# Kernel optimization log

Hardware: AMD Instinct MI355X
Metric: run time of the kernel (lower is better)

Reference implementation:

```python
import jax, jax.numpy as jnp
import numpy as np

B, S, D, H = 128, 256, 256, 8   # graphs, nodes/graph, dim_h, heads
N = B * S
E = 524288
DH = D // H
BN_EPS = 1e-5

def _bn(v, g, b):
    # BatchNorm1d forward with batch statistics (biased var), eval-dropout model
    m = v.mean(0)
    var = v.var(0)
    return (v - m) * jax.lax.rsqrt(var + BN_EPS) * g + b

def setup_inputs() -> dict:
    key = jax.random.key(0)
    ks = jax.random.split(key, 40)
    x = jax.random.normal(ks[0], (N, D), jnp.float32)
    src = jax.random.randint(ks[1], (E,), 0, N)
    dst = (src // S) * S + jax.random.randint(ks[2], (E,), 0, S)  # intra-graph edges
    edge_index = jnp.stack([src, dst]).astype(jnp.int64)
    def lin(k, i, o):
        return (jax.random.normal(k, (i, o), jnp.float32) / np.float32(np.sqrt(i)))
    inp = {
        'x': x, 'edge_index': edge_index,
        'W_gcn': lin(ks[3], D, D), 'b_gcn': jnp.zeros((D,), jnp.float32),
        'W_gin1': lin(ks[4], D, D), 'b_gin1': jnp.zeros((D,), jnp.float32),
        'W_gin2': lin(ks[5], D, D), 'b_gin2': jnp.zeros((D,), jnp.float32),
        'g_kv': jnp.ones((D,), jnp.float32), 'be_kv': jnp.zeros((D,), jnp.float32),
        'Wq1': lin(ks[6], D, D), 'bq1': jnp.zeros((D,), jnp.float32),
        'Wq2': lin(ks[7], D, D), 'bq2': jnp.zeros((D,), jnp.float32),
        'Wq_a': lin(ks[8], D, D), 'bq_a': jnp.zeros((D,), jnp.float32),
        'Wk_a': lin(ks[9], D, D), 'bk_a': jnp.zeros((D,), jnp.float32),
        'Wv_a': lin(ks[10], D, D), 'bv_a': jnp.zeros((D,), jnp.float32),
        'Wo_a': lin(ks[11], D, D), 'bo_a': jnp.zeros((D,), jnp.float32),
        'g_attn': jnp.ones((D,), jnp.float32), 'be_attn': jnp.zeros((D,), jnp.float32),
        'Wf1': lin(ks[12], D, 2 * D), 'bf1': jnp.zeros((2 * D,), jnp.float32),
        'Wf2': lin(ks[13], 2 * D, D), 'bf2': jnp.zeros((D,), jnp.float32),
        'g2': jnp.ones((D,), jnp.float32), 'be2': jnp.zeros((D,), jnp.float32),
    }
    return inp

def _forward(x, edge_index,
             W_gcn, b_gcn, W_gin1, b_gin1, W_gin2, b_gin2, g_kv, be_kv,
             Wq1, bq1, Wq2, bq2,
             Wq_a, bq_a, Wk_a, bk_a, Wv_a, bv_a, Wo_a, bo_a, g_attn, be_attn,
             Wf1, bf1, Wf2, bf2, g2, be2):
    row, col = edge_index[0], edge_index[1]
    h_in1 = x

    # ---- expert 0: GCNConv (add self loops + symmetric norm) ----
    loops = jnp.arange(N, dtype=row.dtype)
    row2 = jnp.concatenate([row, loops])
    col2 = jnp.concatenate([col, loops])
    deg = jax.ops.segment_sum(jnp.ones_like(row2, jnp.float32), col2, num_segments=N)
    dinv = jnp.where(deg > 0, jax.lax.rsqrt(deg), 0.0)
    norm = dinv[row2] * dinv[col2]                     # [E+N]
    xw = x @ W_gcn                                      # [N, D]
    h_gcn = jax.ops.segment_sum(norm[:, None] * xw[row2], col2, num_segments=N) + b_gcn
    e0 = _bn(h_gcn, g_kv, be_kv)

    # ---- expert 1: GINConv (eps=0, sum aggregation, 2-layer MLP) ----
    agg = jax.ops.segment_sum(x[row], col, num_segments=N)
    h_gin = jax.nn.relu((x + agg) @ W_gin1 + b_gin1) @ W_gin2 + b_gin2
    e1 = _bn(h_gin, g_kv, be_kv)

    # ---- global expert normalization (torch .std -> unbiased) ----
    allo = jnp.concatenate([e0, e1], axis=0)
    gm = allo.mean()
    gs = jnp.std(allo, ddof=1)
    e0 = (e0 - gm) / (gs + 1e-8)
    e1 = (e1 - gm) / (gs + 1e-8)

    # ---- uniform routing & kv residual mix ----
    kv = 0.5 * e0 + 0.5 * e1 + 0.1 * h_in1              # [N, D]

    # ---- dense batching (equal-sized graphs -> pure reshape, full mask) ----
    q_dense = h_in1.reshape(B, S, D)
    kv_dense = kv.reshape(B, S, D)

    # ---- q projection MLP ----
    q_dense = jax.nn.relu(q_dense @ Wq1 + bq1) @ Wq2 + bq2

    # ---- multihead attention (batch_first, no padding) ----
    qh = (q_dense @ Wq_a + bq_a).reshape(B, S, H, DH)
    kh = (kv_dense @ Wk_a + bk_a).reshape(B, S, H, DH)
    vh = (kv_dense @ Wv_a + bv_a).reshape(B, S, H, DH)
    scores = jnp.einsum('bqhd,bkhd->bhqk', qh, kh) / np.float32(np.sqrt(DH))
    attn = jax.nn.softmax(scores, axis=-1)
    o = jnp.einsum('bhqk,bkhd->bqhd', attn, vh).reshape(B, S, D)
    h_attn = (o @ Wo_a + bo_a).reshape(N, D)

    # ---- residual + norm + FFN block ----
    h = _bn(h_in1 + h_attn, g_attn, be_attn)
    h_ff = jax.nn.relu(h @ Wf1 + bf1) @ Wf2 + bf2
    h = _bn(h + h_ff, g2, be2)
    return h

def reference(x, edge_index,
              W_gcn, b_gcn, W_gin1, b_gin1, W_gin2, b_gin2, g_kv, be_kv,
              Wq1, bq1, Wq2, bq2,
              Wq_a, bq_a, Wk_a, bk_a, Wv_a, bv_a, Wo_a, bo_a, g_attn, be_attn,
              Wf1, bf1, Wf2, bf2, g2, be2):
    return _forward(x, edge_index,
                    W_gcn, b_gcn, W_gin1, b_gin1, W_gin2, b_gin2, g_kv, be_kv,
                    Wq1, bq1, Wq2, bq2,
                    Wq_a, bq_a, Wk_a, bk_a, Wv_a, bv_a, Wo_a, bo_a, g_attn, be_attn,
                    Wf1, bf1, Wf2, bf2, g2, be2)
```

## Files before the change

### kernel.cpp

```cpp
#include <hip/hip_runtime.h>
#include <hip/hip_bf16.h>

typedef __hip_bfloat16 bf16;
typedef __attribute__((ext_vector_type(8))) short short8;
typedef __attribute__((ext_vector_type(4))) short short4v;
typedef __attribute__((ext_vector_type(4))) float f32x4;
typedef __attribute__((ext_vector_type(4))) int i32x4;

#define N_ 32768
#define D_ 256
#define S_ 256
#define B_ 128
#define E_ 524288

static __device__ __forceinline__ f32x4 mfma16(short8 a, short8 b, f32x4 c) {
  return __builtin_amdgcn_mfma_f32_16x16x32_bf16(a, b, c, 0, 0, 0);
}
static __device__ __forceinline__ f32x4 fzero4() {
  f32x4 z; z[0] = 0.f; z[1] = 0.f; z[2] = 0.f; z[3] = 0.f; return z;
}
static __device__ __forceinline__ float bits2f(short s) {
  unsigned u = ((unsigned)(unsigned short)s) << 16;
  return __builtin_bit_cast(float, u);
}
static __device__ __forceinline__ short f2bits(float f) {
  bf16 b = __float2bfloat16(f);
  return __builtin_bit_cast(short, b);
}
static __device__ __forceinline__ float tof(float x) { return x; }
static __device__ __forceinline__ float tof(bf16 x) { return __bfloat162float(x); }

#define GLOAD_LDS16(G, L) __builtin_amdgcn_global_load_lds( \
    (const __attribute__((address_space(1))) void*)(G),     \
    (__attribute__((address_space(3))) void*)(L), 16, 0, 0)

template<int F>
__global__ __launch_bounds__(256)
void gemm_bt(const bf16* __restrict__ A, const bf16* __restrict__ Bt,
             const float* __restrict__ bias, const float* __restrict__ biasB,
             const void* __restrict__ resid,
             float* __restrict__ Cf, bf16* __restrict__ Cb,
             float* __restrict__ Sp, float* __restrict__ SSp,
             int M, int Nc, int K, long bsA, long bsB, long bsC)
{
  __shared__ __align__(16) bf16 lA[128 * 32];
  __shared__ __align__(16) bf16 lB[128 * 32];
  __shared__ float sS[2][128], sSS[2][128];
  const int z = blockIdx.z;
  const bf16* Ab = A + (long)z * bsA;
  const bf16* Bb = Bt + (long)z * bsB;
  const int m0 = blockIdx.x * 128, n0 = blockIdx.y * 128;
  const int tid = threadIdx.x;
  const int lane = tid & 63;
  const int w = tid >> 6, wr = w >> 1, wc = w & 1;
  const int g = lane >> 4, r = lane & 15, ko = g * 8;
  const int srow = lane >> 2, skw = (lane & 3) * 8;

  f32x4 acc[4][4];
  for (int i = 0; i < 4; i++) for (int j = 0; j < 4; j++) acc[i][j] = fzero4();

  for (int k0 = 0; k0 < K; k0 += 32) {
    __syncthreads();
    for (int i = 0; i < 2; i++) {
      const int c = w * 2 + i;
      GLOAD_LDS16(Ab + (long)(m0 + c * 16 + srow) * K + k0 + skw, lA + c * 512);
      GLOAD_LDS16(Bb + (long)(n0 + c * 16 + srow) * K + k0 + skw, lB + c * 512);
    }
    __syncthreads();
    short8 af[4], bfv[4];
    for (int mi = 0; mi < 4; mi++)
      af[mi] = *(const short8*)&lA[(wr * 64 + mi * 16 + r) * 32 + ko];
    for (int ni = 0; ni < 4; ni++)
      bfv[ni] = *(const short8*)&lB[(wc * 64 + ni * 16 + r) * 32 + ko];
    for (int mi = 0; mi < 4; mi++)
      for (int ni = 0; ni < 4; ni++)
        acc[mi][ni] = mfma16(af[mi], bfv[ni], acc[mi][ni]);
  }

  float cs[4] = {0, 0, 0, 0}, css[4] = {0, 0, 0, 0};
  for (int mi = 0; mi < 4; mi++) for (int ni = 0; ni < 4; ni++) {
    const int row = m0 + wr * 64 + mi * 16 + g * 4;
    const int col = n0 + wc * 64 + ni * 16 + r;
    float bv = 0.0f;
    if (F & 2) {
      if ((F & 128) && col >= 256) bv = biasB[col - 256];
      else bv = bias[col];
    }
    for (int j = 0; j < 4; j++) {
      long idx = (long)(row + j) * Nc + col;
      float v = acc[mi][ni][j] + bv;
      if (F & 4)  v += ((const float*)resid)[(long)z * bsC + idx];
      if (F & 64) v += bits2f(((const short*)resid)[(long)z * bsC + idx]);
      if (F & 1)  v = fmaxf(v, 0.0f);
      if (F & 32) { cs[ni] += v; css[ni] += v * v; }
      if (F & 8)  Cf[(long)z * bsC + idx] = v;
      if (F & 16) Cb[(long)z * bsC + idx] = __float2bfloat16(v);
    }
  }
  if (F & 32) {
    for (int ni = 0; ni < 4; ni++) {
      cs[ni]  += __shfl_xor(cs[ni], 16);  cs[ni]  += __shfl_xor(cs[ni], 32);
      css[ni] += __shfl_xor(css[ni], 16); css[ni] += __shfl_xor(css[ni], 32);
    }
    if (lane < 16) {
      for (int ni = 0; ni < 4; ni++) {
        sS[wr][wc * 64 + ni * 16 + lane]  = cs[ni];
        sSS[wr][wc * 64 + ni * 16 + lane] = css[ni];
      }
    }
    __syncthreads();
    if (tid < 128) {
      atomicAdd(&Sp[n0 + tid],  sS[0][tid] + sS[1][tid]);
      atomicAdd(&SSp[n0 + tid], sSS[0][tid] + sSS[1][tid]);
    }
  }
}

template<int STAGES, bool STATS>
__global__ __launch_bounds__(512)
void mlp_fused(const bf16* __restrict__ A,
               const bf16* __restrict__ B1, const float* __restrict__ b1,
               const bf16* __restrict__ B2, const float* __restrict__ b2,
               const bf16* __restrict__ B3, const float* __restrict__ b3,
               bf16* __restrict__ C, float* __restrict__ Sp, float* __restrict__ SSp)
{
  __shared__ __align__(16) bf16 lA[64 * 32];
  __shared__ __align__(16) bf16 lB[256 * 32];
  __shared__ __align__(16) bf16 lC[64 * 256];
  char* lCc = (char*)lC;
  const int tid = threadIdx.x;
  const int lane = tid & 63;
  const int w = tid >> 6;
  const int mh = w >> 2, nq = w & 3;
  const int g = lane >> 4, r = lane & 15, ko = g * 8;
  const int m0 = blockIdx.x * 64;

  f32x4 acc[2][4];
  for (int i = 0; i < 2; i++) for (int j = 0; j < 4; j++) acc[i][j] = fzero4();

  for (int k0 = 0; k0 < 256; k0 += 32) {
    __syncthreads();
    if (tid < 256)
      GLOAD_LDS16(A + (long)(m0 + (tid >> 2)) * 256 + k0 + (tid & 3) * 8,
                  lA + w * 512);
    GLOAD_LDS16(B1 + (long)(tid >> 2) * 256 + k0 + (tid & 3) * 8,
                lB + w * 512);
    GLOAD_LDS16(B1 + (long)((tid + 512) >> 2) * 256 + k0 + ((tid + 512) & 3) * 8,
                lB + w * 512 + 4096);
    __syncthreads();
    short8 af[2], bfv[4];
    for (int mi = 0; mi < 2; mi++)
      af[mi] = *(const short8*)&lA[(mh * 32 + mi * 16 + r) * 32 + ko];
    for (int ni = 0; ni < 4; ni++)
      bfv[ni] = *(const short8*)&lB[(nq * 64 + ni * 16 + r) * 32 + ko];
    for (int mi = 0; mi < 2; mi++)
      for (int ni = 0; ni < 4; ni++)
        acc[mi][ni] = mfma16(af[mi], bfv[ni], acc[mi][ni]);
  }
  for (int mi = 0; mi < 2; mi++) for (int ni = 0; ni < 4; ni++) {
    const int col = nq * 64 + ni * 16 + r;
    const float bv = b1[col];
    for (int j = 0; j < 4; j++) {
      const int row = mh * 32 + mi * 16 + g * 4 + j;
      float v = fmaxf(acc[mi][ni][j] + bv, 0.0f);
      *(short*)(lCc + ((row * 512 + col * 2) ^ ((row & 7) << 4))) = f2bits(v);
    }
  }
  __syncthreads();

  const bf16* Bs = B2;
  for (int s = 1; s < STAGES; s++) {
    for (int i = 0; i < 2; i++) for (int j = 0; j < 4; j++) acc[i][j] = fzero4();
    for (int k0 = 0; k0 < 256; k0 += 32) {
      __syncthreads();
      GLOAD_LDS16(Bs + (long)(tid >> 2) * 256 + k0 + (tid & 3) * 8,
                  lB + w * 512);
      GLOAD_LDS16(Bs + (long)((tid + 512) >> 2) * 256 + k0 + ((tid + 512) & 3) * 8,
                  lB + w * 512 + 4096);
      __syncthreads();
      short8 af[2], bfv[4];
      for (int mi = 0; mi < 2; mi++) {
        const int row = mh * 32 + mi * 16 + r;
        af[mi] = *(const short8*)(lCc +
                  ((row * 512 + (k0 + ko) * 2) ^ ((row & 7) << 4)));
      }
      for (int ni = 0; ni < 4; ni++)
        bfv[ni] = *(const short8*)&lB[(nq * 64 + ni * 16 + r) * 32 + ko];
      for (int mi = 0; mi < 2; mi++)
        for (int ni = 0; ni < 4; ni++)
          acc[mi][ni] = mfma16(af[mi], bfv[ni], acc[mi][ni]);
    }
    if (s < STAGES - 1) {
      __syncthreads();
      for (int mi = 0; mi < 2; mi++) for (int ni = 0; ni < 4; ni++) {
        const int col = nq * 64 + ni * 16 + r;
        const float bv = b2[col];
        for (int j = 0; j < 4; j++) {
          const int row = mh * 32 + mi * 16 + g * 4 + j;
          float v = acc[mi][ni][j] + bv;
          *(short*)(lCc + ((row * 512 + col * 2) ^ ((row & 7) << 4))) = f2bits(v);
        }
      }
      __syncthreads();
      Bs = B3;
    }
  }

  const float* bf_ = (STAGES == 3) ? b3 : b2;
  float cs[4] = {0, 0, 0, 0}, css[4] = {0, 0, 0, 0};
  for (int mi = 0; mi < 2; mi++) for (int ni = 0; ni < 4; ni++) {
    const int col = nq * 64 + ni * 16 + r;
    const float bv = bf_[col];
    for (int j = 0; j < 4; j++) {
      const int row = mh * 32 + mi * 16 + g * 4 + j;
      float v = acc[mi][ni][j] + bv;
      if (STATS) { cs[ni] += v; css[ni] += v * v; }
      C[(long)(m0 + row) * 256 + col] = __float2bfloat16(v);
    }
  }
  if (STATS) {
    for (int ni = 0; ni < 4; ni++) {
      cs[ni]  += __shfl_xor(cs[ni], 16);  cs[ni]  += __shfl_xor(cs[ni], 32);
      css[ni] += __shfl_xor(css[ni], 16); css[ni] += __shfl_xor(css[ni], 32);
    }
    __syncthreads();
    float* sS = (float*)lC;
    if (lane < 16) {
      for (int ni = 0; ni < 4; ni++) {
        sS[mh * 256 + nq * 64 + ni * 16 + lane] = cs[ni];
        sS[512 + mh * 256 + nq * 64 + ni * 16 + lane] = css[ni];
      }
    }
    __syncthreads();
    if (tid < 256) {
      atomicAdd(&Sp[tid],  sS[tid] + sS[256 + tid]);
      atomicAdd(&SSp[tid], sS[512 + tid] + sS[768 + tid]);
    }
  }
}

__global__ __launch_bounds__(256, 2)
void attn_k(const bf16* __restrict__ qh, const bf16* __restrict__ kh,
            const bf16* __restrict__ vh, bf16* __restrict__ ob, int ks)
{
  const int h = blockIdx.x, qhf = blockIdx.y, b = blockIdx.z;
  const int tid = threadIdx.x, lane = tid & 63, w = tid >> 6;
  const int g = lane >> 4, r = lane & 15, ko = g * 8;
  __shared__ __align__(16) bf16 lK[256 * 32];
  __shared__ __align__(16) bf16 lV[32 * 256];
  char* lKc = (char*)lK;
  char* lVc = (char*)lV;

  for (int i = 0; i < 4; i++) {
    int c = tid + i * 256;
    int row = c >> 2, p4 = c & 3;
    short8 v = *(const short8*)(kh + (long)(b * 256 + row) * ks + h * 32 + p4 * 8);
    *(short8*)(lKc + ((row * 64 + p4 * 16) ^ ((row & 7) << 4))) = v;
  }
  for (int i = 0; i < 2; i++) {
    int c = tid + i * 256;
    int sp = c >> 2, part = c & 3;
    const bf16* vp = vh + (long)(b * 256 + 2 * sp) * ks + h * 32 + part * 8;
    short8 va = *(const short8*)(vp);
    short8 vb = *(const short8*)(vp + ks);
    #pragma unroll
    for (int j = 0; j < 8; j++) {
      int dh = part * 8 + j;
      int sw = ((dh & 7) ^ ((dh >> 3) << 1)) & 7;
      unsigned wrd = ((unsigned)(unsigned short)vb[j] << 16) |
                     (unsigned)(unsigned short)va[j];
      *(unsigned*)(lVc + ((dh * 512 + sp * 4) ^ (sw << 4))) = wrd;
    }
  }
  __syncthreads();

  const float c1 = 0.17677669529663687f * 1.4426950408889634f;
  const int idx0 = (((lane >> 4) & 1) * 32 + r) * 4;
  const int idx1 = idx0 + 64;
  const bool selhi = lane >= 32;

  for (int mc = 0; mc < 2; mc++) {
    const long qbase = (long)b * 256 + qhf * 128 + w * 32 + mc * 16;
    short8 qf = *(const short8*)(qh + (qbase + r) * 256 + h * 32 + ko);
    f32x4 sc[16];
    __builtin_amdgcn_s_setprio(1);
    #pragma unroll
    for (int nc = 0; nc < 16; nc++) {
      int row = nc * 16 + r;
      short8 kf = *(const short8*)(lKc + ((row * 64 + g * 16) ^ ((r & 7) << 4)));
      sc[nc] = mfma16(kf, qf, fzero4());
    }
    __builtin_amdgcn_s_setprio(0);
    f32x4 m4 = sc[0];
    #pragma unroll
    for (int nc = 1; nc < 16; nc++)
      for (int j = 0; j < 4; j++) m4[j] = fmaxf(m4[j], sc[nc][j]);
    float mx = fmaxf(fmaxf(m4[0], m4[1]), fmaxf(m4[2], m4[3]));
    mx = fmaxf(mx, __shfl_xor(mx, 16));
    mx = fmaxf(mx, __shfl_xor(mx, 32));
    const float mxc = mx * c1;
    f32x4 s4 = fzero4();
    #pragma unroll
    for (int nc = 0; nc < 16; nc++)
      for (int j = 0; j < 4; j++) {
        float p = exp2f(fmaf(sc[nc][j], c1, -mxc));
        sc[nc][j] = p; s4[j] += p;
      }
    float sum = s4[0] + s4[1] + s4[2] + s4[3];
    sum += __shfl_xor(sum, 16);
    sum += __shfl_xor(sum, 32);
    const float invs = 1.0f / sum;
    f32x4 oa[2]; oa[0] = fzero4(); oa[1] = fzero4();
    __builtin_amdgcn_s_setprio(1);
    #pragma unroll
    for (int kc = 0; kc < 8; kc++) {
      int pkA0, pkA1, pkB0, pkB1;
      {
        const f32x4 pa = sc[2 * kc], pb = sc[2 * kc + 1];
        unsigned a0 = (unsigned short)f2bits(pa[0] * invs);
        unsigned a1 = (unsigned short)f2bits(pa[1] * invs);
        unsigned a2 = (unsigned short)f2bits(pa[2] * invs);
        unsigned a3 = (unsigned short)f2bits(pa[3] * invs);
        unsigned b0 = (unsigned short)f2bits(pb[0] * invs);
        unsigned b1 = (unsigned short)f2bits(pb[1] * invs);
        unsigned b2 = (unsigned short)f2bits(pb[2] * invs);
        unsigned b3 = (unsigned short)f2bits(pb[3] * invs);
        pkA0 = (int)((a1 << 16) | a0);
        pkA1 = (int)((a3 << 16) | a2);
        pkB0 = (int)((b1 << 16) | b0);
        pkB1 = (int)((b3 << 16) | b2);
      }
      int A0 = __builtin_amdgcn_ds_bpermute(idx0, pkA0);
      int A1 = __builtin_amdgcn_ds_bpermute(idx0, pkA1);
      int B0 = __builtin_amdgcn_ds_bpermute(idx0, pkB0);
      int B1 = __builtin_amdgcn_ds_bpermute(idx0, pkB1);
      int C0 = __builtin_amdgcn_ds_bpermute(idx1, pkA0);
      int C1 = __builtin_amdgcn_ds_bpermute(idx1, pkA1);
      int D0 = __builtin_amdgcn_ds_bpermute(idx1, pkB0);
      int D1 = __builtin_amdgcn_ds_bpermute(idx1, pkB1);
      i32x4 av;
      av[0] = selhi ? B0 : A0;
      av[1] = selhi ? B1 : A1;
      av[2] = selhi ? D0 : C0;
      av[3] = selhi ? D1 : C1;
      short8 af = __builtin_bit_cast(short8, av);
      #pragma unroll
      for (int n = 0; n < 2; n++) {
        int dh = n * 16 + r;
        int sw = ((dh & 7) ^ ((dh >> 3) << 1)) & 7;
        short8 bv = *(const short8*)(lVc + ((dh * 512 + kc * 64 + g * 16) ^ (sw << 4)));
        oa[n] = mfma16(af, bv, oa[n]);
      }
    }
    __builtin_amdgcn_s_setprio(0);
    #pragma unroll
    for (int n = 0; n < 2; n++)
      for (int j = 0; j < 4; j++)
        ob[(qbase + g * 4 + j) * 256 + h * 32 + n * 16 + r] =
          __float2bfloat16(oa[n][j]);
  }
}

template<typename TIN>
__global__ __launch_bounds__(256)
void transpose_cast_k(const TIN* __restrict__ in, bf16* __restrict__ out,
                      int in_rs, int out_rs, long zhi, long out_zs)
{
  __shared__ float tile[32][33];
  const int z = blockIdx.z;
  const long ioff = (long)z * zhi;
  const long ooff = (long)z * out_zs;
  const int tx = threadIdx.x, ty = threadIdx.y;
  const int c = blockIdx.x * 32 + tx;
  const int rb = blockIdx.y * 32;
  for (int i = 0; i < 4; i++)
    tile[ty + i * 8][tx] = tof(in[ioff + (long)(rb + ty + i * 8) * in_rs + c]);
  __syncthreads();
  const int oc = rb + tx;
  const int orb = blockIdx.x * 32;
  for (int i = 0; i < 4; i++)
    out[ooff + (long)(orb + ty + i * 8) * out_rs + oc] =
      __float2bfloat16(tile[tx][ty + i * 8]);
}

__global__ __launch_bounds__(256)
void xprep_k(const float* __restrict__ x, bf16* __restrict__ xb,
             bf16* __restrict__ xT)
{
  __shared__ float tile[32][33];
  const int z = blockIdx.z;
  const long ioff = (long)z * 65536;
  const int tx = threadIdx.x, ty = threadIdx.y;
  const int c = blockIdx.x * 32 + tx;
  const int rb = blockIdx.y * 32;
  for (int i = 0; i < 4; i++) {
    float v = x[ioff + (long)(rb + ty + i * 8) * 256 + c];
    tile[ty + i * 8][tx] = v;
    xb[ioff + (long)(rb + ty + i * 8) * 256 + c] = __float2bfloat16(v);
  }
  __syncthreads();
  const int oc = rb + tx;
  const int orb = blockIdx.x * 32;
  for (int i = 0; i < 4; i++)
    xT[ioff + (long)(orb + ty + i * 8) * 256 + oc] =
      __float2bfloat16(tile[tx][ty + i * 8]);
}

__global__ __launch_bounds__(256)
void w9t_k(const float* w0, const float* w1, const float* w2, const float* w3,
           const float* w4, const float* w5, const float* w6, const float* w7,
           const float* w8, bf16* __restrict__ out)
{
  __shared__ float tile[32][33];
  const float* srcs[9] = {w0, w1, w2, w3, w4, w5, w6, w7, w8};
  const int wi = blockIdx.z;
  const float* in = srcs[wi];
  bf16* o = out + (long)wi * 65536;
  const int tx = threadIdx.x, ty = threadIdx.y;
  const int c = blockIdx.x * 32 + tx;
  const int rb = blockIdx.y * 32;
  for (int i = 0; i < 4; i++)
    tile[ty + i * 8][tx] = in[(rb + ty + i * 8) * 256 + c];
  __syncthreads();
  const int oc = rb + tx;
  const int orb = blockIdx.x * 32;
  for (int i = 0; i < 4; i++)
    o[(orb + ty + i * 8) * 256 + oc] = __float2bfloat16(tile[tx][ty + i * 8]);
}

__global__ __launch_bounds__(256)
void edge_cnt_k(const int* __restrict__ ei, unsigned* __restrict__ cnt)
{
  int e = blockIdx.x * 256 + threadIdx.x;
  int src = ei[e], dst = ei[E_ + e];
  long idx = ((long)(src >> 8) * 256 + (dst & 255)) * 256 + (src & 255);
  atomicAdd(&cnt[idx >> 2], 1u << ((idx & 3) * 8));
}

__global__ __launch_bounds__(256)
void deg_k(const unsigned* __restrict__ cnt, float* __restrict__ dinv)
{
  int rid = blockIdx.x * 16 + (threadIdx.x >> 4);
  int l16 = threadIdx.x & 15;
  uint4 v = ((const uint4*)(cnt + (long)rid * 64))[l16];
  unsigned s = 0;
  s += (v.x & 0xFF) + ((v.x >> 8) & 0xFF) + ((v.x >> 16) & 0xFF) + (v.x >> 24);
  s += (v.y & 0xFF) + ((v.y >> 8) & 0xFF) + ((v.y >> 16) & 0xFF) + (v.y >> 24);
  s += (v.z & 0xFF) + ((v.z >> 8) & 0xFF) + ((v.z >> 16) & 0xFF) + (v.z >> 24);
  s += (v.w & 0xFF) + ((v.w >> 8) & 0xFF) + ((v.w >> 16) & 0xFF) + (v.w >> 24);
  s += __shfl_xor(s, 1); s += __shfl_xor(s, 2);
  s += __shfl_xor(s, 4); s += __shfl_xor(s, 8);
  if (l16 == 0) dinv[rid] = rsqrtf((float)s + 1.0f);
}

__global__ __launch_bounds__(256)
void adj_derive_k(const unsigned* __restrict__ cnt, const float* __restrict__ dinv,
                  bf16* __restrict__ gin, bf16* __restrict__ gcn)
{
  long wi = (long)blockIdx.x * 256 + threadIdx.x;
  unsigned cw = cnt[wi];
  long i = wi * 4;
  float cv[4] = {(float)(cw & 0xFF), (float)((cw >> 8) & 0xFF),
                 (float)((cw >> 16) & 0xFF), (float)(cw >> 24)};
  long row = i >> 8;
  int g = (int)(row >> 8), dst = (int)(row & 255);
  int src0 = (int)(i & 255);
  float dd = dinv[row];
  const float* ds = dinv + (long)g * 256 + src0;
  short4v oi, oc;
  for (int j = 0; j < 4; j++) {
    float gv = cv[j] * dd * ds[j];
    if (src0 + j == dst) gv += dd * dd;
    oi[j] = f2bits(cv[j]);
    oc[j] = f2bits(gv);
  }
  *(short4v*)(gin + i) = oi;
  *(short4v*)(gcn + i) = oc;
}

__global__ __launch_bounds__(256)
void expert_stats_k(const float* __restrict__ S0, const float* __restrict__ SS0,
                    const float* __restrict__ S1, const float* __restrict__ SS1,
                    const float* __restrict__ gkv, const float* __restrict__ bkv,
                    float* __restrict__ kA, float* __restrict__ kB,
                    float* __restrict__ kC)
{
  const int d = threadIdx.x;
  const float invN = 1.0f / 32768.0f;
  float m0 = S0[d] * invN, v0 = SS0[d] * invN - m0 * m0;
  float a0 = gkv[d] * rsqrtf(v0 + 1e-5f), c0 = bkv[d] - m0 * a0;
  float m1 = S1[d] * invN, v1 = SS1[d] * invN - m1 * m1;
  float a1 = gkv[d] * rsqrtf(v1 + 1e-5f), c1 = bkv[d] - m1 * a1;
  float gsum = a0 * S0[d] + 32768.0f * c0 + a1 * S1[d] + 32768.0f * c1;
  float gss  = a0 * a0 * SS0[d] + 2.0f * a0 * c0 * S0[d] + 32768.0f * c0 * c0
             + a1 * a1 * SS1[d] + 2.0f * a1 * c1 * S1[d] + 32768.0f * c1 * c1;
  __shared__ float r1[256], r2[256];
  r1[d] = gsum; r2[d] = gss;
  __syncthreads();
  for (int s = 128; s > 0; s >>= 1) {
    if (d < s) { r1[d] += r1[d + s]; r2[d] += r2[d + s]; }
    __syncthreads();
  }
  const float cntall = 16777216.0f;
  float tg = r1[0], tss = r2[0];
  float gm = tg / cntall;
  float var = (tss - tg * tg / cntall) / (cntall - 1.0f);
  float gs = sqrtf(fmaxf(var, 0.f)) + 1e-8f;
  kA[d] = 0.5f * a0 / gs;
  kB[d] = 0.5f * a1 / gs;
  kC[d] = 0.5f * (c0 + c1 - 2.0f * gm) / gs;
}

__global__ __launch_bounds__(256)
void kv_mix_k(const bf16* __restrict__ hgcn, const bf16* __restrict__ hgin,
              const bf16* __restrict__ xb, const float* __restrict__ kA,
              const float* __restrict__ kB, const float* __restrict__ kC,
              bf16* __restrict__ kv)
{
  long i = ((long)blockIdx.x * 256 + threadIdx.x) * 8;
  int d0 = (int)(i & 255);
  short8 a = *(const short8*)(hgcn + i);
  short8 b = *(const short8*)(hgin + i);
  short8 c = *(const short8*)(xb + i);
  short8 o;
  for (int j = 0; j < 8; j++) {
    int d = d0 + j;
    float v = kA[d] * bits2f(a[j]) + kB[d] * bits2f(b[j]) + kC[d] + 0.1f * bits2f(c[j]);
    o[j] = f2bits(v);
  }
  *(short8*)(kv + i) = o;
}

template<int MODE>
__global__ __launch_bounds__(256)
void bn_apply_k(const bf16* __restrict__ in, const float* __restrict__ S,
                const float* __restrict__ SSq, const float* __restrict__ gg,
                const float* __restrict__ bb, float* __restrict__ outf,
                bf16* __restrict__ outb)
{
  long i = ((long)blockIdx.x * 256 + threadIdx.x) * 8;
  int d0 = (int)(i & 255);
  short8 v = *(const short8*)(in + i);
  const float invN = 1.0f / 32768.0f;
  float4 o0, o1; short8 o8;
  for (int j = 0; j < 8; j++) {
    int d = d0 + j;
    float m = S[d] * invN;
    float var = SSq[d] * invN - m * m;
    float a = gg[d] * rsqrtf(var + 1e-5f);
    float c = bb[d] - m * a;
    float o = a * bits2f(v[j]) + c;
    if (MODE & 1) { if (j < 4) (&o0.x)[j] = o; else (&o1.x)[j - 4] = o; }
    if (MODE & 2) o8[j] = f2bits(o);
  }
  if (MODE & 1) { *(float4*)(outf + i) = o0; *(float4*)(outf + i + 4) = o1; }
  if (MODE & 2) *(short8*)(outb + i) = o8;
}

static constexpr size_t OFF_S0 = 0, OFF_SS0 = 1024, OFF_S1 = 2048, OFF_SS1 = 3072;
static constexpr size_t OFF_S2 = 4096, OFF_SS2 = 5120, OFF_S3 = 6144, OFF_SS3 = 7168;
static constexpr size_t OFF_KA = 8192, OFF_KB = 9216, OFF_KC = 10240;
static constexpr size_t OFF_CNT = 16384;
static constexpr size_t CNT_BYTES = (size_t)B_ * S_ * S_;
static constexpr size_t ZERO_BYTES = OFF_CNT + CNT_BYTES;
static constexpr size_t OFF_DINV = OFF_CNT + (size_t)B_ * S_ * S_ * 2;
static constexpr size_t OFF_W = OFF_DINV + 131072;
static constexpr size_t NDB2 = (size_t)N_ * D_ * 2;
static constexpr size_t OFF_ADJGINB = OFF_W + 1703936;
static constexpr size_t OFF_ADJGCNB = OFF_ADJGINB + NDB2;
static constexpr size_t OFF_XB   = OFF_ADJGCNB + NDB2;
static constexpr size_t OFF_XT   = OFF_XB + NDB2;
static constexpr size_t OFF_AGG  = OFF_XT + NDB2;
static constexpr size_t OFF_GIN  = OFF_AGG + NDB2;
static constexpr size_t OFF_KV   = OFF_GIN + NDB2;
static constexpr size_t OFF_HGCN = OFF_KV + NDB2;
static constexpr size_t OFF_HGIN = OFF_HGCN + NDB2;

extern "C" void kernel_launch(void* const* d_in, const int* in_sizes, int n_in,
                              void* d_out, int out_size, void* d_ws, size_t ws_size,
                              hipStream_t stream)
{
  (void)in_sizes; (void)n_in; (void)out_size; (void)ws_size;
  const float* x      = (const float*)d_in[0];
  const int*   ei     = (const int*)d_in[1];
  const float* W_gcn  = (const float*)d_in[2];
  const float* b_gcn  = (const float*)d_in[3];
  const float* W_gin1 = (const float*)d_in[4];
  const float* b_gin1 = (const float*)d_in[5];
  const float* W_gin2 = (const float*)d_in[6];
  const float* b_gin2 = (const float*)d_in[7];
  const float* g_kv   = (const float*)d_in[8];
  const float* be_kv  = (const float*)d_in[9];
  const float* Wq1    = (const float*)d_in[10];
  const float* bq1    = (const float*)d_in[11];
  const float* Wq2    = (const float*)d_in[12];
  const float* bq2    = (const float*)d_in[13];
  const float* Wq_a   = (const float*)d_in[14];
  const float* bq_a   = (const float*)d_in[15];
  const float* Wk_a   = (const float*)d_in[16];
  const float* bk_a   = (const float*)d_in[17];
  const float* Wv_a   = (const float*)d_in[18];
  const float* bv_a   = (const float*)d_in[19];
  const float* Wo_a   = (const float*)d_in[20];
  const float* bo_a   = (const float*)d_in[21];
  const float* g_attn = (const float*)d_in[22];
  const float* be_attn= (const float*)d_in[23];
  const float* Wf1    = (const float*)d_in[24];
  const float* bf1    = (const float*)d_in[25];
  const float* Wf2    = (const float*)d_in[26];
  const float* bf2    = (const float*)d_in[27];
  const float* g2     = (const float*)d_in[28];
  const float* be2    = (const float*)d_in[29];

  char* ws = (char*)d_ws;
  float* S0  = (float*)(ws + OFF_S0);  float* SS0 = (float*)(ws + OFF_SS0);
  float* S1  = (float*)(ws + OFF_S1);  float* SS1 = (float*)(ws + OFF_SS1);
  float* S2  = (float*)(ws + OFF_S2);  float* SS2 = (float*)(ws + OFF_SS2);
  float* S3  = (float*)(ws + OFF_S3);  float* SS3 = (float*)(ws + OFF_SS3);
  float* kA  = (float*)(ws + OFF_KA);  float* kB  = (float*)(ws + OFF_KB);
  float* kC  = (float*)(ws + OFF_KC);
  unsigned* cntA = (unsigned*)(ws + OFF_CNT);
  float* dinv = (float*)(ws + OFF_DINV);
  bf16* wT = (bf16*)(ws + OFF_W);
  bf16 *WgcnT = wT,            *Wgin1T = wT + 65536,  *Wgin2T = wT + 131072;
  bf16 *Wq1T  = wT + 196608,   *Wq2T   = wT + 262144, *WqaT   = wT + 327680;
  bf16 *WkaT  = wT + 393216,   *WvaT   = wT + 458752, *WoaT   = wT + 524288;
  bf16 *Wf1T  = wT + 589824,   *Wf2T   = wT + 720896;
  (void)WvaT;
  bf16* adjGINb = (bf16*)(ws + OFF_ADJGINB);
  bf16* adjGCNb = (bf16*)(ws + OFF_ADJGCNB);
  bf16* xb    = (bf16*)(ws + OFF_XB);
  bf16* xT    = (bf16*)(ws + OFF_XT);
  bf16* aggb  = (bf16*)(ws + OFF_AGG);
  bf16* gin_in= (bf16*)(ws + OFF_GIN);
  bf16* kv_bf = (bf16*)(ws + OFF_KV);
  bf16* hgcnb = (bf16*)(ws + OFF_HGCN);
  bf16* hginb = (bf16*)(ws + OFF_HGIN);
  bf16* qhb    = adjGINb;
  bf16* khvb   = aggb;
  bf16* ob     = hginb;
  bf16* tbufb  = (bf16*)(ws + OFF_CNT);
  bf16* hb     = xb;
  bf16* f1b    = adjGINb;
  bf16* t2b    = (bf16*)(ws + OFF_CNT);
  float* outp  = (float*)d_out;

  hipMemsetAsync(d_ws, 0, ZERO_BYTES, stream);

  dim3 tb(32, 8);
  w9t_k<<<dim3(8, 8, 9), tb, 0, stream>>>(W_gcn, W_gin1, W_gin2, Wq1, Wq2,
                                          Wq_a, Wk_a, Wv_a, Wo_a, wT);
  transpose_cast_k<float><<<dim3(16, 8, 1), tb, 0, stream>>>(Wf1, Wf1T, 512, 256, 0, 0);
  transpose_cast_k<float><<<dim3(8, 16, 1), tb, 0, stream>>>(Wf2, Wf2T, 256, 512, 0, 0);
  xprep_k<<<dim3(8, 8, 128), tb, 0, stream>>>(x, xb, xT);
  edge_cnt_k<<<2048, 256, 0, stream>>>(ei, cntA);
  deg_k<<<2048, 256, 0, stream>>>(cntA, dinv);
  adj_derive_k<<<8192, 256, 0, stream>>>(cntA, dinv, adjGINb, adjGCNb);
  gemm_bt<16><<<dim3(2, 2, 128), 256, 0, stream>>>(adjGCNb, xT, nullptr, nullptr,
      nullptr, nullptr, aggb, nullptr, nullptr, 256, 256, 256, 65536, 65536, 65536);
  gemm_bt<80><<<dim3(2, 2, 128), 256, 0, stream>>>(adjGINb, xT, nullptr, nullptr,
      xb, nullptr, gin_in, nullptr, nullptr, 256, 256, 256, 65536, 65536, 65536);
  gemm_bt<50><<<dim3(256, 2, 1), 256, 0, stream>>>(aggb, WgcnT, b_gcn, nullptr,
      nullptr, nullptr, hgcnb, S0, SS0, N_, 256, 256, 0, 0, 0);
  mlp_fused<2, true><<<512, 512, 0, stream>>>(gin_in, Wgin1T, b_gin1,
      Wgin2T, b_gin2, nullptr, nullptr, hginb, S1, SS1);
  expert_stats_k<<<1, 256, 0, stream>>>(S0, SS0, S1, SS1, g_kv, be_kv, kA, kB, kC);
  kv_mix_k<<<4096, 256, 0, stream>>>(hgcnb, hginb, xb, kA, kB, kC, kv_bf);
  mlp_fused<3, false><<<512, 512, 0, stream>>>(xb, Wq1T, bq1,
      Wq2T, bq2, WqaT, bq_a, qhb, nullptr, nullptr);
  gemm_bt<146><<<dim3(256, 4, 1), 256, 0, stream>>>(kv_bf, WkaT, bk_a, bv_a,
      nullptr, nullptr, khvb, nullptr, nullptr, N_, 512, 256, 0, 0, 0);
  attn_k<<<dim3(8, 2, 128), 256, 0, stream>>>(qhb, khvb, khvb + 256, ob, 512);
  gemm_bt<114><<<dim3(256, 2, 1), 256, 0, stream>>>(ob, WoaT, bo_a, nullptr,
      xb, nullptr, tbufb, S2, SS2, N_, 256, 256, 0, 0, 0);
  bn_apply_k<2><<<4096, 256, 0, stream>>>(tbufb, S2, SS2, g_attn, be_attn, nullptr, hb);
  gemm_bt<19><<<dim3(256, 4, 1), 256, 0, stream>>>(hb, Wf1T, bf1, nullptr,
      nullptr, nullptr, f1b, nullptr, nullptr, N_, 512, 256, 0, 0, 0);
  gemm_bt<114><<<dim3(256, 2, 1), 256, 0, stream>>>(f1b, Wf2T, bf2, nullptr,
      hb, nullptr, t2b, S3, SS3, N_, 256, 512, 0, 0, 0);
  bn_apply_k<1><<<4096, 256, 0, stream>>>(t2b, S3, SS3, g2, be2, outp, nullptr);
}
```

Measured before the change: 319.5 us.

## Fuse adjacency aggregation into expert MLP chains and merge into one launch

Replaces the separate per-graph adjacency GEMMs (GCN and GIN aggregation) and their follow-on weight GEMMs with a single fused kernel. Each block runs the aggregation and the MLP chain with intermediates held in LDS, and a third block range computes the query MLP chain in the same launch. Weight transpose kernels are also merged into one launch. This removes the round-trip of the aggregated intermediates through global memory and several kernel launches. In exchange the grid is heterogeneous, the blocks do uneven amounts of work, and workspace aliasing changes because qhb now lives in the count buffer.

```diff
diff --git a/kernel.cpp b/kernel.cpp
--- a/kernel.cpp
+++ b/kernel.cpp
@@ -27,8 +27,6 @@
   bf16 b = __float2bfloat16(f);
   return __builtin_bit_cast(short, b);
 }
-static __device__ __forceinline__ float tof(float x) { return x; }
-static __device__ __forceinline__ float tof(bf16 x) { return __bfloat162float(x); }
 
 #define GLOAD_LDS16(G, L) __builtin_amdgcn_global_load_lds( \
     (const __attribute__((address_space(1))) void*)(G),     \
@@ -116,24 +114,21 @@
   }
 }
 
-template<int STAGES, bool STATS>
-__global__ __launch_bounds__(512)
-void mlp_fused(const bf16* __restrict__ A,
-               const bf16* __restrict__ B1, const float* __restrict__ b1,
-               const bf16* __restrict__ B2, const float* __restrict__ b2,
-               const bf16* __restrict__ B3, const float* __restrict__ b3,
-               bf16* __restrict__ C, float* __restrict__ Sp, float* __restrict__ SSp)
-{
-  __shared__ __align__(16) bf16 lA[64 * 32];
-  __shared__ __align__(16) bf16 lB[256 * 32];
-  __shared__ __align__(16) bf16 lC[64 * 256];
+template<int NS, int EP1, int EP2, bool STATS>
+static __device__ __forceinline__ void mlp_body(
+    const bf16* __restrict__ A, const bf16* __restrict__ B1,
+    const bf16* __restrict__ B2, const bf16* __restrict__ B3,
+    const float* __restrict__ bEp1, const float* __restrict__ bEp2,
+    const float* __restrict__ bFin, const bf16* __restrict__ resid,
+    bf16* __restrict__ out, float* __restrict__ Sp, float* __restrict__ SSp,
+    bf16* lA, bf16* lB, bf16* lC)
+{
   char* lCc = (char*)lC;
   const int tid = threadIdx.x;
   const int lane = tid & 63;
   const int w = tid >> 6;
   const int mh = w >> 2, nq = w & 3;
   const int g = lane >> 4, r = lane & 15, ko = g * 8;
-  const int m0 = blockIdx.x * 64;
 
   f32x4 acc[2][4];
   for (int i = 0; i < 2; i++) for (int j = 0; j < 4; j++) acc[i][j] = fzero4();
@@ -141,10 +136,8 @@
   for (int k0 = 0; k0 < 256; k0 += 32) {
     __syncthreads();
     if (tid < 256)
-      GLOAD_LDS16(A + (long)(m0 + (tid >> 2)) * 256 + k0 + (tid & 3) * 8,
-                  lA + w * 512);
-    GLOAD_LDS16(B1 + (long)(tid >> 2) * 256 + k0 + (tid & 3) * 8,
-                lB + w * 512);
+      GLOAD_LDS16(A + (long)(tid >> 2) * 256 + k0 + (tid & 3) * 8, lA + w * 512);
+    GLOAD_LDS16(B1 + (long)(tid >> 2) * 256 + k0 + (tid & 3) * 8, lB + w * 512);
     GLOAD_LDS16(B1 + (long)((tid + 512) >> 2) * 256 + k0 + ((tid + 512) & 3) * 8,
                 lB + w * 512 + 4096);
     __syncthreads();
@@ -159,22 +152,23 @@
   }
   for (int mi = 0; mi < 2; mi++) for (int ni = 0; ni < 4; ni++) {
     const int col = nq * 64 + ni * 16 + r;
-    const float bv = b1[col];
+    const float bv = (EP1 & 1) ? bEp1[col] : 0.0f;
     for (int j = 0; j < 4; j++) {
       const int row = mh * 32 + mi * 16 + g * 4 + j;
-      float v = fmaxf(acc[mi][ni][j] + bv, 0.0f);
+      float v = acc[mi][ni][j] + bv;
+      if (EP1 & 4) v += bits2f(__builtin_bit_cast(short, resid[(long)row * 256 + col]));
+      if (EP1 & 2) v = fmaxf(v, 0.0f);
       *(short*)(lCc + ((row * 512 + col * 2) ^ ((row & 7) << 4))) = f2bits(v);
     }
   }
   __syncthreads();
 
-  const bf16* Bs = B2;
-  for (int s = 1; s < STAGES; s++) {
+  for (int s = 2; s <= NS; s++) {
+    const bf16* Bs = (s == 2) ? B2 : B3;
     for (int i = 0; i < 2; i++) for (int j = 0; j < 4; j++) acc[i][j] = fzero4();
     for (int k0 = 0; k0 < 256; k0 += 32) {
       __syncthreads();
-      GLOAD_LDS16(Bs + (long)(tid >> 2) * 256 + k0 + (tid & 3) * 8,
-                  lB + w * 512);
+      GLOAD_LDS16(Bs + (long)(tid >> 2) * 256 + k0 + (tid & 3) * 8, lB + w * 512);
       GLOAD_LDS16(Bs + (long)((tid + 512) >> 2) * 256 + k0 + ((tid + 512) & 3) * 8,
                   lB + w * 512 + 4096);
       __syncthreads();
@@ -190,32 +184,31 @@
         for (int ni = 0; ni < 4; ni++)
           acc[mi][ni] = mfma16(af[mi], bfv[ni], acc[mi][ni]);
     }
-    if (s < STAGES - 1) {
+    if (s < NS) {
       __syncthreads();
       for (int mi = 0; mi < 2; mi++) for (int ni = 0; ni < 4; ni++) {
         const int col = nq * 64 + ni * 16 + r;
-        const float bv = b2[col];
+        const float bv = (EP2 & 1) ? bEp2[col] : 0.0f;
         for (int j = 0; j < 4; j++) {
           const int row = mh * 32 + mi * 16 + g * 4 + j;
           float v = acc[mi][ni][j] + bv;
+          if (EP2 & 2) v = fmaxf(v, 0.0f);
           *(short*)(lCc + ((row * 512 + col * 2) ^ ((row & 7) << 4))) = f2bits(v);
         }
       }
       __syncthreads();
-      Bs = B3;
-    }
-  }
-
-  const float* bf_ = (STAGES == 3) ? b3 : b2;
+    }
+  }
+
   float cs[4] = {0, 0, 0, 0}, css[4] = {0, 0, 0, 0};
   for (int mi = 0; mi < 2; mi++) for (int ni = 0; ni < 4; ni++) {
     const int col = nq * 64 + ni * 16 + r;
-    const float bv = bf_[col];
+    const float bv = bFin[col];
     for (int j = 0; j < 4; j++) {
       const int row = mh * 32 + mi * 16 + g * 4 + j;
       float v = acc[mi][ni][j] + bv;
       if (STATS) { cs[ni] += v; css[ni] += v * v; }
-      C[(long)(m0 + row) * 256 + col] = __float2bfloat16(v);
+      out[(long)row * 256 + col] = __float2bfloat16(v);
     }
   }
   if (STATS) {
@@ -236,6 +229,43 @@
       atomicAdd(&Sp[tid],  sS[tid] + sS[256 + tid]);
       atomicAdd(&SSp[tid], sS[512 + tid] + sS[768 + tid]);
     }
+  }
+}
+
+__global__ __launch_bounds__(512)
+void fused3_k(const bf16* __restrict__ adjGCNb, const bf16* __restrict__ adjGINb,
+              const bf16* __restrict__ xT, const bf16* __restrict__ xb,
+              const bf16* __restrict__ WgcnT, const bf16* __restrict__ Wgin1T,
+              const bf16* __restrict__ Wgin2T, const bf16* __restrict__ Wq1T,
+              const bf16* __restrict__ Wq2T, const bf16* __restrict__ WqaT,
+              const float* __restrict__ b_gcn, const float* __restrict__ b_gin1,
+              const float* __restrict__ b_gin2, const float* __restrict__ bq1,
+              const float* __restrict__ bq2, const float* __restrict__ bq_a,
+              bf16* __restrict__ hgcnb, bf16* __restrict__ hginb,
+              bf16* __restrict__ qhb,
+              float* __restrict__ S0, float* __restrict__ SS0,
+              float* __restrict__ S1, float* __restrict__ SS1)
+{
+  __shared__ __align__(16) bf16 lA[64 * 32];
+  __shared__ __align__(16) bf16 lB[256 * 32];
+  __shared__ __align__(16) bf16 lC[64 * 256];
+  const int bid = blockIdx.x;
+  if (bid < 512) {
+    const long g = bid >> 2;
+    mlp_body<2, 0, 0, true>(adjGCNb + (long)bid * 16384, xT + g * 65536,
+        WgcnT, nullptr, nullptr, nullptr, b_gcn, nullptr,
+        hgcnb + (long)bid * 16384, S0, SS0, lA, lB, lC);
+  } else if (bid < 1024) {
+    const int sub = bid - 512;
+    const long g = sub >> 2;
+    mlp_body<3, 4, 3, true>(adjGINb + (long)sub * 16384, xT + g * 65536,
+        Wgin1T, Wgin2T, nullptr, b_gin1, b_gin2, xb + (long)sub * 16384,
+        hginb + (long)sub * 16384, S1, SS1, lA, lB, lC);
+  } else {
+    const int sub = bid - 1024;
+    mlp_body<3, 3, 1, false>(xb + (long)sub * 16384, Wq1T, Wq2T, WqaT,
+        bq1, bq2, bq_a, nullptr, qhb + (long)sub * 16384, nullptr, nullptr,
+        lA, lB, lC);
   }
 }
 
@@ -361,25 +391,39 @@
   }
 }
 
-template<typename TIN>
-__global__ __launch_bounds__(256)
-void transpose_cast_k(const TIN* __restrict__ in, bf16* __restrict__ out,
-                      int in_rs, int out_rs, long zhi, long out_zs)
+__global__ __launch_bounds__(256)
+void wprep_k(const float* w0, const float* w1, const float* w2, const float* w3,
+             const float* w4, const float* w5, const float* w6, const float* w7,
+             const float* w8, const float* wf1, const float* wf2,
+             bf16* __restrict__ wT)
 {
   __shared__ float tile[32][33];
-  const int z = blockIdx.z;
-  const long ioff = (long)z * zhi;
-  const long ooff = (long)z * out_zs;
+  const float* srcs[9] = {w0, w1, w2, w3, w4, w5, w6, w7, w8};
+  const int bid = blockIdx.x;
+  const float* in; bf16* out; int in_rs, out_rs, bx, by;
+  if (bid < 576) {
+    int wi = bid >> 6, t = bid & 63;
+    in = srcs[wi]; out = wT + (long)wi * 65536;
+    in_rs = 256; out_rs = 256; bx = t & 7; by = t >> 3;
+  } else if (bid < 704) {
+    int t = bid - 576;
+    in = wf1; out = wT + 589824;
+    in_rs = 512; out_rs = 256; bx = t & 15; by = t >> 4;
+  } else {
+    int t = bid - 704;
+    in = wf2; out = wT + 720896;
+    in_rs = 256; out_rs = 512; bx = t & 7; by = t >> 3;
+  }
   const int tx = threadIdx.x, ty = threadIdx.y;
-  const int c = blockIdx.x * 32 + tx;
-  const int rb = blockIdx.y * 32;
+  const int c = bx * 32 + tx;
+  const int rb = by * 32;
   for (int i = 0; i < 4; i++)
-    tile[ty + i * 8][tx] = tof(in[ioff + (long)(rb + ty + i * 8) * in_rs + c]);
+    tile[ty + i * 8][tx] = in[(long)(rb + ty + i * 8) * in_rs + c];
   __syncthreads();
   const int oc = rb + tx;
-  const int orb = blockIdx.x * 32;
+  const int orb = bx * 32;
   for (int i = 0; i < 4; i++)
-    out[ooff + (long)(orb + ty + i * 8) * out_rs + oc] =
+    out[(long)(orb + ty + i * 8) * out_rs + oc] =
       __float2bfloat16(tile[tx][ty + i * 8]);
 }
 
@@ -404,28 +448,6 @@
   for (int i = 0; i < 4; i++)
     xT[ioff + (long)(orb + ty + i * 8) * 256 + oc] =
       __float2bfloat16(tile[tx][ty + i * 8]);
-}
-
-__global__ __launch_bounds__(256)
-void w9t_k(const float* w0, const float* w1, const float* w2, const float* w3,
-           const float* w4, const float* w5, const float* w6, const float* w7,
-           const float* w8, bf16* __restrict__ out)
-{
-  __shared__ float tile[32][33];
-  const float* srcs[9] = {w0, w1, w2, w3, w4, w5, w6, w7, w8};
-  const int wi = blockIdx.z;
-  const float* in = srcs[wi];
-  bf16* o = out + (long)wi * 65536;
-  const int tx = threadIdx.x, ty = threadIdx.y;
-  const int c = blockIdx.x * 32 + tx;
-  const int rb = blockIdx.y * 32;
-  for (int i = 0; i < 4; i++)
-    tile[ty + i * 8][tx] = in[(rb + ty + i * 8) * 256 + c];
-  __syncthreads();
-  const int oc = rb + tx;
-  const int orb = blockIdx.x * 32;
-  for (int i = 0; i < 4; i++)
-    o[(orb + ty + i * 8) * 256 + oc] = __float2bfloat16(tile[tx][ty + i * 8]);
 }
 
 __global__ __launch_bounds__(256)
@@ -624,20 +646,17 @@
   bf16* wT = (bf16*)(ws + OFF_W);
   bf16 *WgcnT = wT,            *Wgin1T = wT + 65536,  *Wgin2T = wT + 131072;
   bf16 *Wq1T  = wT + 196608,   *Wq2T   = wT + 262144, *WqaT   = wT + 327680;
-  bf16 *WkaT  = wT + 393216,   *WvaT   = wT + 458752, *WoaT   = wT + 524288;
+  bf16 *WkaT  = wT + 393216,   *WoaT   = wT + 524288;
   bf16 *Wf1T  = wT + 589824,   *Wf2T   = wT + 720896;
-  (void)WvaT;
   bf16* adjGINb = (bf16*)(ws + OFF_ADJGINB);
   bf16* adjGCNb = (bf16*)(ws + OFF_ADJGCNB);
   bf16* xb    = (bf16*)(ws + OFF_XB);
   bf16* xT    = (bf16*)(ws + OFF_XT);
-  bf16* aggb  = (bf16*)(ws + OFF_AGG);
-  bf16* gin_in= (bf16*)(ws + OFF_GIN);
   bf16* kv_bf = (bf16*)(ws + OFF_KV);
   bf16* hgcnb = (bf16*)(ws + OFF_HGCN);
   bf16* hginb = (bf16*)(ws + OFF_HGIN);
-  bf16* qhb    = adjGINb;
-  bf16* khvb   = aggb;
+  bf16* qhb    = (bf16*)(ws + OFF_CNT);
+  bf16* khvb   = (bf16*)(ws + OFF_AGG);
   bf16* ob     = hginb;
   bf16* tbufb  = (bf16*)(ws + OFF_CNT);
   bf16* hb     = xb;
@@ -648,26 +667,18 @@
   hipMemsetAsync(d_ws, 0, ZERO_BYTES, stream);
 
   dim3 tb(32, 8);
-  w9t_k<<<dim3(8, 8, 9), tb, 0, stream>>>(W_gcn, W_gin1, W_gin2, Wq1, Wq2,
-                                          Wq_a, Wk_a, Wv_a, Wo_a, wT);
-  transpose_cast_k<float><<<dim3(16, 8, 1), tb, 0, stream>>>(Wf1, Wf1T, 512, 256, 0, 0);
-  transpose_cast_k<float><<<dim3(8, 16, 1), tb, 0, stream>>>(Wf2, Wf2T, 256, 512, 0, 0);
+  wprep_k<<<832, tb, 0, stream>>>(W_gcn, W_gin1, W_gin2, Wq1, Wq2,
+                                  Wq_a, Wk_a, Wv_a, Wo_a, Wf1, Wf2, wT);
   xprep_k<<<dim3(8, 8, 128), tb, 0, stream>>>(x, xb, xT);
   edge_cnt_k<<<2048, 256, 0, stream>>>(ei, cntA);
   deg_k<<<2048, 256, 0, stream>>>(cntA, dinv);
   adj_derive_k<<<8192, 256, 0, stream>>>(cntA, dinv, adjGINb, adjGCNb);
-  gemm_bt<16><<<dim3(2, 2, 128), 256, 0, stream>>>(adjGCNb, xT, nullptr, nullptr,
-      nullptr, nullptr, aggb, nullptr, nullptr, 256, 256, 256, 65536, 65536, 65536);
-  gemm_bt<80><<<dim3(2, 2, 128), 256, 0, stream>>>(adjGINb, xT, nullptr, nullptr,
-      xb, nullptr, gin_in, nullptr, nullptr, 256, 256, 256, 65536, 65536, 65536);
-  gemm_bt<50><<<dim3(256, 2, 1), 256, 0, stream>>>(aggb, WgcnT, b_gcn, nullptr,
-      nullptr, nullptr, hgcnb, S0, SS0, N_, 256, 256, 0, 0, 0);
-  mlp_fused<2, true><<<512, 512, 0, stream>>>(gin_in, Wgin1T, b_gin1,
-      Wgin2T, b_gin2, nullptr, nullptr, hginb, S1, SS1);
+  fused3_k<<<1536, 512, 0, stream>>>(adjGCNb, adjGINb, xT, xb,
+      WgcnT, Wgin1T, Wgin2T, Wq1T, Wq2T, WqaT,
+      b_gcn, b_gin1, b_gin2, bq1, bq2, bq_a,
+      hgcnb, hginb, qhb, S0, SS0, S1, SS1);
   expert_stats_k<<<1, 256, 0, stream>>>(S0, SS0, S1, SS1, g_kv, be_kv, kA, kB, kC);
   kv_mix_k<<<4096, 256, 0, stream>>>(hgcnb, hginb, xb, kA, kB, kC, kv_bf);
-  mlp_fused<3, false><<<512, 512, 0, stream>>>(xb, Wq1T, bq1,
-      Wq2T, bq2, WqaT, bq_a, qhb, nullptr, nullptr);
   gemm_bt<146><<<dim3(256, 4, 1), 256, 0, stream>>>(kv_bf, WkaT, bk_a, bv_a,
       nullptr, nullptr, khvb, nullptr, nullptr, N_, 512, 256, 0, 0, 0);
   attn_k<<<dim3(8, 2, 128), 256, 0, stream>>>(qhb, khvb, khvb + 256, ob, 512);
```

Result: no change. 320.7 us (+0.4%).
